# Kernel optimization log

Measured on AMD Instinct MI355X. Metric: run time of the kernel, lower is better.

Reference implementation:

```python
import jax, jax.numpy as jnp
import numpy as np
from jax import lax

B, C, H, W, NH = 16, 512, 32, 32, 8
HC = C // NH  # head channels = 64


def setup_inputs() -> dict:
    key = jax.random.key(0)
    ks = jax.random.split(key, 8)
    rn = lambda i, shape, scale: jax.random.normal(ks[i], shape, jnp.float32) * scale
    return dict(
        image=jax.random.normal(ks[0], (B, C, H, W), jnp.float32),
        watermark=jax.random.normal(ks[1], (B, C, H, W), jnp.float32),
        img_ln_w=jnp.ones((C, H, W), jnp.float32),
        img_ln_b=jnp.zeros((C, H, W), jnp.float32),
        wm_ln_w=jnp.ones((C, H, W), jnp.float32),
        wm_ln_b=jnp.zeros((C, H, W), jnp.float32),
        img_pw_w=rn(2, (3 * C, C), 0.02),
        img_pw_b=jnp.zeros((3 * C,), jnp.float32),
        img_dw_w=rn(3, (3 * C, 3, 3, 3), 0.1),
        img_dw_b=jnp.zeros((3 * C,), jnp.float32),
        wm_pw_w=rn(4, (3 * C, C), 0.02),
        wm_pw_b=jnp.zeros((3 * C,), jnp.float32),
        wm_dw_w=rn(5, (3 * C, 3, 3, 3), 0.1),
        wm_dw_b=jnp.zeros((3 * C,), jnp.float32),
        proj=rn(6, (2 * C, C), 0.02),
    )


def _layernorm(x, w, b, eps=1e-5):
    # LayerNorm over [C,H,W] per sample, elementwise affine of shape [C,H,W]
    mu = jnp.mean(x, axis=(1, 2, 3), keepdims=True)
    var = jnp.mean((x - mu) ** 2, axis=(1, 2, 3), keepdims=True)
    return (x - mu) * lax.rsqrt(var + eps) * w + b


def _dconv_proj(x, pw_w, pw_b, dw_w, dw_b):
    # pointwise 1x1 conv C -> 3C
    x = jnp.einsum('bchw,oc->bohw', x, pw_w) + pw_b[None, :, None, None]
    # depthwise 3x3 conv on 3C channels with groups=C (3 channels per group)
    x = lax.conv_general_dilated(
        x, dw_w, window_strides=(1, 1), padding='SAME',
        dimension_numbers=('NCHW', 'OIHW', 'NCHW'), feature_group_count=C)
    x = x + dw_b[None, :, None, None]
    return jnp.split(x, 3, axis=1)  # Q, K, V each [B,C,H,W]


def reference(image, watermark, img_ln_w, img_ln_b, wm_ln_w, wm_ln_b,
              img_pw_w, img_pw_b, img_dw_w, img_dw_b,
              wm_pw_w, wm_pw_b, wm_dw_w, wm_dw_b, proj):
    img = _layernorm(image, img_ln_w, img_ln_b)
    wm = _layernorm(watermark, wm_ln_w, wm_ln_b)
    Qi, Ki, Vi = _dconv_proj(img, img_pw_w, img_pw_b, img_dw_w, img_dw_b)
    Qw, Kw, Vw = _dconv_proj(wm, wm_pw_w, wm_pw_b, wm_dw_w, wm_dw_b)
    r = lambda t: t.reshape(B, NH, HC, H * W)
    Qi, Ki, Vi, Qw, Kw, Vw = map(r, (Qi, Ki, Vi, Qw, Kw, Vw))
    # NOTE: original code calls F.normalize but discards the result -> no-op.
    Kc = jnp.concatenate([Ki, Kw], axis=2)  # [B,NH,2*HC,HW]
    Vc = jnp.concatenate([Vi, Vw], axis=2)  # [B,NH,2*HC,HW]
    # scores: K_concat @ Q^T over the HW axis -> [B,NH,2*HC,HC], softmax over HC
    Ai = jax.nn.softmax(jnp.einsum('bnkp,bnqp->bnkq', Kc, Qi), axis=-1)
    Aw = jax.nn.softmax(jnp.einsum('bnkp,bnqp->bnkq', Kc, Qw), axis=-1)
    # A^T @ V_concat -> [B,NH,HC,HW]
    img_attn = jnp.einsum('bnkq,bnkp->bnqp', Ai, Vc)
    wm_attn = jnp.einsum('bnkq,bnkp->bnqp', Aw, Vc)
    attn = jnp.concatenate([img_attn, wm_attn], axis=2).reshape(B, 2 * C, H, W)
    # final channel-mixing projection: [B,H,W,2C] @ [2C,C] -> [B,C,H,W]
    return jnp.einsum('bdhw,dc->bchw', attn, proj)
```

## Files before the change

### kernel.cpp

```cpp
#include <hip/hip_runtime.h>
#include <hip/hip_bf16.h>
#include <stdint.h>

#define Bn  16
#define Cch 512
#define C3  1536
#define HWp 1024

typedef __attribute__((ext_vector_type(8))) short bf16x8;
typedef __attribute__((ext_vector_type(4))) float f32x4;

#define DEV static __device__ __forceinline__

DEV float bflo(unsigned u) { return __builtin_bit_cast(float, u << 16); }
DEV float bfhi(unsigned u) { return __builtin_bit_cast(float, u & 0xffff0000u); }
DEV unsigned short f2bf(float f) {
  __hip_bfloat16 h = __float2bfloat16(f);
  return __builtin_bit_cast(unsigned short, h);
}

DEV void async16(__hip_bfloat16* lds, const __hip_bfloat16* g) {
  __builtin_amdgcn_global_load_lds(
      (const __attribute__((address_space(1))) unsigned*)g,
      (__attribute__((address_space(3))) unsigned*)lds, 16, 0, 0);
}

__global__ __launch_bounds__(256) void k_prep_ln(
    const float* __restrict__ img_pw_w, const float* __restrict__ wm_pw_w,
    const float* __restrict__ proj,
    const float* __restrict__ image, const float* __restrict__ watermark,
    __hip_bfloat16* __restrict__ Wpw, __hip_bfloat16* __restrict__ projT,
    float* __restrict__ part)
{
  __shared__ float ls[4], lss[4];
  int blkid = blockIdx.x;
  if (blkid < 8192) {
    int i = blkid * 256 + threadIdx.x;
    const int NW = C3 * Cch;
    if (i < NW)          Wpw[i] = __float2bfloat16(img_pw_w[i]);
    else if (i < 2 * NW) Wpw[i] = __float2bfloat16(wm_pw_w[i - NW]);
    else {
      int j = i - 2 * NW;
      int c = j >> 10, d = j & 1023;
      projT[(size_t)c * 1024 + d] = __float2bfloat16(proj[(size_t)d * 512 + c]);
    }
    return;
  }
  int blk = blkid - 8192;
  int chunk = blk & 63, b = (blk >> 6) & 15, t = blk >> 10;
  const float* x = (t ? watermark : image) + (size_t)b * Cch * HWp + chunk * 8192;
  const float4* xv = (const float4*)x;
  float s = 0.f, ss = 0.f;
#pragma unroll
  for (int i = 0; i < 8; i++) {
    float4 v = xv[threadIdx.x + i * 256];
    s  += v.x + v.y + v.z + v.w;
    ss += v.x * v.x + v.y * v.y + v.z * v.z + v.w * v.w;
  }
#pragma unroll
  for (int off = 32; off; off >>= 1) { s += __shfl_down(s, off); ss += __shfl_down(ss, off); }
  int wv = threadIdx.x >> 6;
  if ((threadIdx.x & 63) == 0) { ls[wv] = s; lss[wv] = ss; }
  __syncthreads();
  if (threadIdx.x == 0) {
    part[blk * 2]     = ls[0] + ls[1] + ls[2] + ls[3];
    part[blk * 2 + 1] = lss[0] + lss[1] + lss[2] + lss[3];
  }
}

__global__ void k_ln_final(const float* __restrict__ part, float* __restrict__ stats)
{
  int i = threadIdx.x;
  if (i < 32) {
    float S = 0.f, SS = 0.f;
    for (int c2 = 0; c2 < 64; c2++) { S += part[(i * 64 + c2) * 2]; SS += part[(i * 64 + c2) * 2 + 1]; }
    const float inv = 1.f / (float)(Cch * HWp);
    float mu  = S * inv;
    float var = SS * inv - mu * mu;
    stats[i]      = mu;
    stats[32 + i] = rsqrtf(var + 1e-5f);
  }
}

__global__ __launch_bounds__(256) void k_norm_t(
    const float* __restrict__ image, const float* __restrict__ watermark,
    const float* __restrict__ img_w, const float* __restrict__ img_b,
    const float* __restrict__ wm_w,  const float* __restrict__ wm_b,
    const float* __restrict__ stats, __hip_bfloat16* __restrict__ xnT)
{
  int blk = blockIdx.x;
  int ct = blk & 15, pt = (blk >> 4) & 15, b = (blk >> 8) & 15, t = blk >> 12;
  int c0 = ct * 32, p0 = pt * 64;
  const float* x   = (t ? watermark : image) + (size_t)b * Cch * HWp;
  const float* wgt = t ? wm_w : img_w;
  const float* bia = t ? wm_b : img_b;
  float mu = stats[t * 16 + b], rstd = stats[32 + t * 16 + b];
  __shared__ float tile[32 * 66];
  int tid = threadIdx.x;
  {
    int c = tid >> 3, s = tid & 7;
    const float* xr = x   + (size_t)(c0 + c) * HWp + p0;
    const float* wr = wgt + (size_t)(c0 + c) * HWp + p0;
    const float* br = bia + (size_t)(c0 + c) * HWp + p0;
#pragma unroll
    for (int j = 0; j < 2; j++) {
      int f = s + j * 8;
      float4 xv = *(const float4*)&xr[f * 4];
      float4 wv = *(const float4*)&wr[f * 4];
      float4 bv = *(const float4*)&br[f * 4];
      float n0 = (xv.x - mu) * rstd * wv.x + bv.x;
      float n1 = (xv.y - mu) * rstd * wv.y + bv.y;
      float n2 = (xv.z - mu) * rstd * wv.z + bv.z;
      float n3 = (xv.w - mu) * rstd * wv.w + bv.w;
      *(float2*)&tile[c * 66 + f * 4]     = make_float2(n0, n1);
      *(float2*)&tile[c * 66 + f * 4 + 2] = make_float2(n2, n3);
    }
  }
  __syncthreads();
  {
    int p = tid >> 2, cq = tid & 3;
    union { unsigned short us[8]; uint4 v4; } pk;
#pragma unroll
    for (int j = 0; j < 8; j++) pk.us[j] = f2bf(tile[(cq * 8 + j) * 66 + p]);
    __hip_bfloat16* dst = xnT + ((size_t)(t * 16 + b)) * HWp * Cch
                        + (size_t)(p0 + p) * Cch + c0 + cq * 8;
    *(uint4*)dst = pk.v4;
  }
}

template<int MI, int Kdim, int Ncols, bool OBF, bool HB>
DEV void gemm_core(const __hip_bfloat16* __restrict__ A,
                   const __hip_bfloat16* __restrict__ Bt,
                   const float* __restrict__ bias, void* __restrict__ Cout)
{
  constexpr int MT = MI * 32;
  __shared__ __hip_bfloat16 As[MT * 64];
  __shared__ __hip_bfloat16 Bs[128 * 64];
  const int tid = threadIdx.x, lane = tid & 63, wv = tid >> 6;
  const int lr = lane & 15, lq = lane >> 4;
  const int wm = (wv >> 1) * (MI * 16), wn = (wv & 1) * 64;
  const int m0 = blockIdx.y * MT, n0 = blockIdx.x * 128;
  f32x4 acc[MI][4] = {};
  const int srow = tid >> 3, sslot = tid & 7;
  const int sseg = (sslot ^ (srow & 7)) * 8;
  for (int k0 = 0; k0 < Kdim; k0 += 64) {
#pragma unroll
    for (int c = 0; c < MI; c++) {
      int row = srow + c * 32;
      async16(&As[row * 64 + sslot * 8], &A[(size_t)(m0 + row) * Kdim + k0 + sseg]);
    }
#pragma unroll
    for (int c = 0; c < 4; c++) {
      int row = srow + c * 32;
      async16(&Bs[row * 64 + sslot * 8], &Bt[(size_t)(n0 + row) * Kdim + k0 + sseg]);
    }
    __syncthreads();
#pragma unroll
    for (int ks = 0; ks < 2; ks++) {
      bf16x8 af[MI], bfr[4];
#pragma unroll
      for (int mi = 0; mi < MI; mi++) {
        int r = wm + mi * 16 + lr;
        af[mi]  = *(const bf16x8*)&As[r * 64 + (((ks * 4 + lq) ^ (lr & 7)) * 8)];
      }
#pragma unroll
      for (int ni = 0; ni < 4; ni++) {
        int r = wn + ni * 16 + lr;
        bfr[ni] = *(const bf16x8*)&Bs[r * 64 + (((ks * 4 + lq) ^ (lr & 7)) * 8)];
      }
#pragma unroll
      for (int mi = 0; mi < MI; mi++)
#pragma unroll
        for (int ni = 0; ni < 4; ni++)
          acc[mi][ni] = __builtin_amdgcn_mfma_f32_16x16x32_bf16(af[mi], bfr[ni], acc[mi][ni], 0, 0, 0);
    }
    __syncthreads();
  }
#pragma unroll
  for (int mi = 0; mi < MI; mi++) {
    int mrow = m0 + wm + mi * 16 + lq * 4;
#pragma unroll
    for (int ni = 0; ni < 4; ni++) {
      int ncol = n0 + wn + ni * 16 + lr;
#pragma unroll
      for (int r = 0; r < 4; r++) {
        float y = acc[mi][ni][r];
        int row = mrow + r;
        if (HB) y += bias[row];
        if (OBF) ((__hip_bfloat16*)Cout)[(size_t)row * Ncols + ncol] = __float2bfloat16(y);
        else     ((float*)Cout)[(size_t)row * Ncols + ncol] = y;
      }
    }
  }
}

__global__ __launch_bounds__(256) void k_pw_gemm(
    const __hip_bfloat16* __restrict__ Wpw, const __hip_bfloat16* __restrict__ xnT,
    const float* __restrict__ img_pw_b, const float* __restrict__ wm_pw_b,
    __hip_bfloat16* __restrict__ Y)
{
  int bz = blockIdx.z, t = bz >> 4;
  gemm_core<4, 512, 1024, true, true>(
      Wpw + (size_t)t * C3 * Cch,
      xnT + (size_t)bz * HWp * Cch,
      t ? wm_pw_b : img_pw_b,
      Y + (size_t)bz * C3 * HWp);
}

__global__ __launch_bounds__(256) void k_proj_gemm(
    const __hip_bfloat16* __restrict__ projT, const __hip_bfloat16* __restrict__ attnT,
    float* __restrict__ out)
{
  int b = blockIdx.z;
  gemm_core<2, 1024, 1024, false, false>(
      projT, attnT + (size_t)b * HWp * 1024, nullptr, out + (size_t)b * Cch * HWp);
}

__global__ __launch_bounds__(256) void k_dw(
    const __hip_bfloat16* __restrict__ Y,
    const float* __restrict__ img_dw_w, const float* __restrict__ img_dw_b,
    const float* __restrict__ wm_dw_w,  const float* __restrict__ wm_dw_b,
    __hip_bfloat16* __restrict__ QKV)
{
  int idx = blockIdx.x * 256 + threadIdx.x;
  int w0 = (idx & 3) * 8;
  int h  = (idx >> 2) & 31;
  int g  = __builtin_amdgcn_readfirstlane((idx >> 7) & 511);
  int tb = __builtin_amdgcn_readfirstlane(idx >> 16);
  int t  = tb >> 4;
  const float* dww = (t ? wm_dw_w : img_dw_w) + g * 81;
  const float* dwb = (t ? wm_dw_b : img_dw_b) + g * 3;
  const __hip_bfloat16* base = Y + ((size_t)tb * C3 + g * 3) * HWp;
  float acc[3][8];
#pragma unroll
  for (int o = 0; o < 3; o++) {
    float bv = dwb[o];
#pragma unroll
    for (int w = 0; w < 8; w++) acc[o][w] = bv;
  }
  const bool mlo = (w0 == 0), mhi = (w0 == 24);
#pragma unroll
  for (int i = 0; i < 3; i++) {
#pragma unroll
    for (int kh = 0; kh < 3; kh++) {
      int hh = h + kh - 1;
      if ((unsigned)hh > 31u) continue;
      const unsigned* up = (const unsigned*)(base + i * HWp + hh * 32 + (w0 - 2));
      float v[12];
#pragma unroll
      for (int d2 = 0; d2 < 6; d2++) { unsigned u = up[d2]; v[d2*2] = bflo(u); v[d2*2+1] = bfhi(u); }
      if (mlo) { v[0] = 0.f; v[1] = 0.f; }
      if (mhi) { v[10] = 0.f; v[11] = 0.f; }
#pragma unroll
      for (int o = 0; o < 3; o++) {
        float wk0 = dww[o*27 + i*9 + kh*3 + 0];
        float wk1 = dww[o*27 + i*9 + kh*3 + 1];
        float wk2 = dww[o*27 + i*9 + kh*3 + 2];
#pragma unroll
        for (int w = 0; w < 8; w++)
          acc[o][w] += v[w + 1] * wk0 + v[w + 2] * wk1 + v[w + 3] * wk2;
      }
    }
  }
#pragma unroll
  for (int o = 0; o < 3; o++) {
    union { unsigned short us[8]; uint4 v4; } pk;
#pragma unroll
    for (int w = 0; w < 8; w++) pk.us[w] = f2bf(acc[o][w]);
    *(uint4*)(QKV + ((size_t)tb * C3 + g * 3 + o) * HWp + h * 32 + w0) = pk.v4;
  }
}

__global__ __launch_bounds__(256) void k_attn_scores(
    const __hip_bfloat16* __restrict__ QKV, __hip_bfloat16* __restrict__ ATg)
{
  int blk = blockIdx.x, kh = blk & 1, m = (blk >> 1) & 1, bn = blk >> 2;
  int b = bn >> 3, nh = bn & 7;
  int tid = threadIdx.x, lane = tid & 63, wv = tid >> 6;
  int lr = lane & 15, lq = lane >> 4;
  const __hip_bfloat16* kb =
      QKV + (((size_t)(kh * 16 + b)) * C3 + 512 + nh * 64 + (wv * 16 + lr)) * HWp + lq * 8;
  const __hip_bfloat16* qbase[4];
#pragma unroll
  for (int qt = 0; qt < 4; qt++)
    qbase[qt] = QKV + (((size_t)(m * 16 + b)) * C3 + nh * 64 + qt * 16 + lr) * HWp + lq * 8;

  f32x4 acc[4] = {};
  for (int p0 = 0; p0 < HWp; p0 += 32) {
    bf16x8 bk = *(const bf16x8*)(kb + p0);
#pragma unroll
    for (int qt = 0; qt < 4; qt++) {
      bf16x8 aq = *(const bf16x8*)(qbase[qt] + p0);
      acc[qt] = __builtin_amdgcn_mfma_f32_16x16x32_bf16(aq, bk, acc[qt], 0, 0, 0);
    }
  }
  __shared__ float S[64][65];
  __shared__ float redmax[4][64];
  __shared__ float redsum[4][64];
  __shared__ __hip_bfloat16 Ash[64][72];
#pragma unroll
  for (int qt = 0; qt < 4; qt++)
#pragma unroll
    for (int r = 0; r < 4; r++)
      S[qt * 16 + lq * 4 + r][wv * 16 + lr] = acc[qt][r];
  __syncthreads();
  int k = tid & 63, sub = tid >> 6;
  float vals[16], mx = -1e30f;
#pragma unroll
  for (int j = 0; j < 16; j++) { vals[j] = S[sub * 16 + j][k]; mx = fmaxf(mx, vals[j]); }
  redmax[sub][k] = mx;
  __syncthreads();
  float M = fmaxf(fmaxf(redmax[0][k], redmax[1][k]), fmaxf(redmax[2][k], redmax[3][k]));
  float ssum = 0.f;
#pragma unroll
  for (int j = 0; j < 16; j++) { vals[j] = __expf(vals[j] - M); ssum += vals[j]; }
  redsum[sub][k] = ssum;
  __syncthreads();
  float inv = 1.f / (redsum[0][k] + redsum[1][k] + redsum[2][k] + redsum[3][k]);
#pragma unroll
  for (int j = 0; j < 16; j++) Ash[sub * 16 + j][k] = __float2bfloat16(vals[j] * inv);
  __syncthreads();
  __hip_bfloat16* outp = ATg + ((size_t)(bn * 2 + m)) * 64 * 128 + kh * 64;
#pragma unroll
  for (int s = 0; s < 2; s++) {
    int id = tid + s * 256, row = id >> 3, seg = (id & 7) * 8;
    *(uint4*)&outp[(size_t)row * 128 + seg] = *(const uint4*)&Ash[row][seg];
  }
}

__global__ __launch_bounds__(256) void k_attn_out(
    const __hip_bfloat16* __restrict__ QKV, const __hip_bfloat16* __restrict__ ATg,
    __hip_bfloat16* __restrict__ attnT)
{
  int blk = blockIdx.x, pc = blk & 3, bn = blk >> 2, b = bn >> 3, nh = bn & 7;
  int tid = threadIdx.x, lane = tid & 63, wv = tid >> 6;
  int lr = lane & 15, lq = lane >> 4;
  __shared__ __hip_bfloat16 ATs[2][64][136];
  __shared__ __hip_bfloat16 VTs[64][136];
#pragma unroll
  for (int m = 0; m < 2; m++) {
    const __hip_bfloat16* src = ATg + ((size_t)(bn * 2 + m)) * 64 * 128;
#pragma unroll
    for (int s = 0; s < 4; s++) {
      int id = tid + s * 256, row = id >> 4, seg = (id & 15) * 8;
      *(uint4*)&ATs[m][row][seg] = *(const uint4*)&src[row * 128 + seg];
    }
  }
  const int vk0 = (tid >> 3) * 4, vps = (tid & 7) * 8;
  for (int ps = 0; ps < 4; ps++) {
    int p0 = pc * 256 + ps * 64;
    __syncthreads();
    union { uint4 v4; unsigned short us[8]; } ld[4];
#pragma unroll
    for (int j = 0; j < 4; j++) {
      int kk = vk0 + j, tk = kk >> 6, hc = kk & 63;
      ld[j].v4 = *(const uint4*)(QKV +
          (((size_t)(tk * 16 + b)) * C3 + 1024 + nh * 64 + hc) * HWp + p0 + vps);
    }
#pragma unroll
    for (int e = 0; e < 8; e++) {
      uint2 w;
      w.x = (unsigned)ld[0].us[e] | ((unsigned)ld[1].us[e] << 16);
      w.y = (unsigned)ld[2].us[e] | ((unsigned)ld[3].us[e] << 16);
      *(uint2*)&VTs[vps + e][vk0] = w;
    }
    __syncthreads();
#pragma unroll
    for (int m = 0; m < 2; m++) {
      f32x4 oacc[4] = {};
#pragma unroll
      for (int ks = 0; ks < 4; ks++) {
        bf16x8 bv = *(const bf16x8*)&VTs[wv * 16 + lr][ks * 32 + lq * 8];
#pragma unroll
        for (int qt = 0; qt < 4; qt++) {
          bf16x8 av = *(const bf16x8*)&ATs[m][qt * 16 + lr][ks * 32 + lq * 8];
          oacc[qt] = __builtin_amdgcn_mfma_f32_16x16x32_bf16(av, bv, oacc[qt], 0, 0, 0);
        }
      }
#pragma unroll
      for (int qt = 0; qt < 4; qt++) {
        int q = qt * 16 + lq * 4;
        int d = nh * 128 + m * 64 + q;
        int p = p0 + wv * 16 + lr;
        union { unsigned short us[4]; uint2 v2; } pk;
#pragma unroll
        for (int r = 0; r < 4; r++) pk.us[r] = f2bf(oacc[qt][r]);
        *(uint2*)&attnT[((size_t)b * HWp + p) * 1024 + d] = pk.v2;
      }
    }
  }
}

extern "C" void kernel_launch(void* const* d_in, const int* in_sizes, int n_in,
                              void* d_out, int out_size, void* d_ws, size_t ws_size,
                              hipStream_t stream)
{
  (void)in_sizes; (void)n_in; (void)out_size; (void)ws_size;
  const float* image     = (const float*)d_in[0];
  const float* watermark = (const float*)d_in[1];
  const float* img_ln_w  = (const float*)d_in[2];
  const float* img_ln_b  = (const float*)d_in[3];
  const float* wm_ln_w   = (const float*)d_in[4];
  const float* wm_ln_b   = (const float*)d_in[5];
  const float* img_pw_w  = (const float*)d_in[6];
  const float* img_pw_b  = (const float*)d_in[7];
  const float* img_dw_w  = (const float*)d_in[8];
  const float* img_dw_b  = (const float*)d_in[9];
  const float* wm_pw_w   = (const float*)d_in[10];
  const float* wm_pw_b   = (const float*)d_in[11];
  const float* wm_dw_w   = (const float*)d_in[12];
  const float* wm_dw_b   = (const float*)d_in[13];
  const float* proj      = (const float*)d_in[14];

  char* ws = (char*)d_ws;
  __hip_bfloat16* Wpw    = (__hip_bfloat16*)(ws + 0);
  __hip_bfloat16* projT  = (__hip_bfloat16*)(ws + 3145728);
  float*          lnpart = (float*)(ws + 4194304);
  float*          stats  = (float*)(ws + 4210688);
  __hip_bfloat16* xnT    = (__hip_bfloat16*)(ws + 5242880);
  __hip_bfloat16* attnT  = xnT;
  __hip_bfloat16* Y      = (__hip_bfloat16*)(ws + 41943040);
  __hip_bfloat16* ATg    = Y;
  __hip_bfloat16* QKV    = (__hip_bfloat16*)(ws + 142606336);

  k_prep_ln<<<10240, 256, 0, stream>>>(img_pw_w, wm_pw_w, proj, image, watermark,
                                       Wpw, projT, lnpart);
  k_ln_final<<<1, 64, 0, stream>>>(lnpart, stats);
  k_norm_t<<<8192, 256, 0, stream>>>(image, watermark, img_ln_w, img_ln_b,
                                     wm_ln_w, wm_ln_b, stats, xnT);
  dim3 gpw(8, 12, 32);
  k_pw_gemm<<<gpw, 256, 0, stream>>>(Wpw, xnT, img_pw_b, wm_pw_b, Y);
  k_dw<<<8192, 256, 0, stream>>>(Y, img_dw_w, img_dw_b, wm_dw_w, wm_dw_b, QKV);
  k_attn_scores<<<512, 256, 0, stream>>>(QKV, ATg);
  k_attn_out<<<512, 256, 0, stream>>>(QKV, ATg, attnT);
  dim3 gpj(8, 8, 16);
  k_proj_gemm<<<gpj, 256, 0, stream>>>(projT, attnT, (float*)d_out);
}
```

Measured before the change: 364.3 us.

## Fuse attention score softmax with output GEMM and fold LN stats into normalize

Merges the attention scores/softmax kernel and the attention-output kernel into one kernel. Each block computes the full 128-key score matrix for its query set and keeps the softmax weights in shared memory, so the global ATg round trip and one launch go away. The price is that each block recomputes the full score GEMM for its half of the positions, duplicating that work across the two halves. Separately, the single-block LN-finalize kernel is removed and every normalize block reduces the 64 partial sums itself, saving a serialized tiny launch at the cost of redundant reductions.

```diff
diff --git a/kernel.cpp b/kernel.cpp
--- a/kernel.cpp
+++ b/kernel.cpp
@@ -68,25 +68,11 @@
   }
 }
 
-__global__ void k_ln_final(const float* __restrict__ part, float* __restrict__ stats)
-{
-  int i = threadIdx.x;
-  if (i < 32) {
-    float S = 0.f, SS = 0.f;
-    for (int c2 = 0; c2 < 64; c2++) { S += part[(i * 64 + c2) * 2]; SS += part[(i * 64 + c2) * 2 + 1]; }
-    const float inv = 1.f / (float)(Cch * HWp);
-    float mu  = S * inv;
-    float var = SS * inv - mu * mu;
-    stats[i]      = mu;
-    stats[32 + i] = rsqrtf(var + 1e-5f);
-  }
-}
-
 __global__ __launch_bounds__(256) void k_norm_t(
     const float* __restrict__ image, const float* __restrict__ watermark,
     const float* __restrict__ img_w, const float* __restrict__ img_b,
     const float* __restrict__ wm_w,  const float* __restrict__ wm_b,
-    const float* __restrict__ stats, __hip_bfloat16* __restrict__ xnT)
+    const float* __restrict__ part, __hip_bfloat16* __restrict__ xnT)
 {
   int blk = blockIdx.x;
   int ct = blk & 15, pt = (blk >> 4) & 15, b = (blk >> 8) & 15, t = blk >> 12;
@@ -94,9 +80,23 @@
   const float* x   = (t ? watermark : image) + (size_t)b * Cch * HWp;
   const float* wgt = t ? wm_w : img_w;
   const float* bia = t ? wm_b : img_b;
-  float mu = stats[t * 16 + b], rstd = stats[32 + t * 16 + b];
+  __shared__ float stt[2];
+  int tid = threadIdx.x;
+  if (tid < 64) {
+    float2 pr = ((const float2*)part)[t * 1024 + b * 64 + tid];
+    float s = pr.x, ss = pr.y;
+#pragma unroll
+    for (int off = 32; off; off >>= 1) { s += __shfl_down(s, off); ss += __shfl_down(ss, off); }
+    if (tid == 0) {
+      const float inv = 1.f / (float)(Cch * HWp);
+      float mu = s * inv;
+      float var = ss * inv - mu * mu;
+      stt[0] = mu; stt[1] = rsqrtf(var + 1e-5f);
+    }
+  }
+  __syncthreads();
+  float mu = stt[0], rstd = stt[1];
   __shared__ float tile[32 * 66];
-  int tid = threadIdx.x;
   {
     int c = tid >> 3, s = tid & 7;
     const float* xr = x   + (size_t)(c0 + c) * HWp + p0;
@@ -271,84 +271,69 @@
   }
 }
 
-__global__ __launch_bounds__(256) void k_attn_scores(
-    const __hip_bfloat16* __restrict__ QKV, __hip_bfloat16* __restrict__ ATg)
-{
-  int blk = blockIdx.x, kh = blk & 1, m = (blk >> 1) & 1, bn = blk >> 2;
+__global__ __launch_bounds__(256) void k_attn(
+    const __hip_bfloat16* __restrict__ QKV, __hip_bfloat16* __restrict__ attnT)
+{
+  int blk = blockIdx.x, ph = blk & 1, m = (blk >> 1) & 1, bn = blk >> 2;
   int b = bn >> 3, nh = bn & 7;
   int tid = threadIdx.x, lane = tid & 63, wv = tid >> 6;
   int lr = lane & 15, lq = lane >> 4;
-  const __hip_bfloat16* kb =
-      QKV + (((size_t)(kh * 16 + b)) * C3 + 512 + nh * 64 + (wv * 16 + lr)) * HWp + lq * 8;
+
+  const __hip_bfloat16* kb[2];
+#pragma unroll
+  for (int kt = 0; kt < 2; kt++)
+    kb[kt] = QKV + (((size_t)(kt * 16 + b)) * C3 + 512 + nh * 64 + (wv * 16 + lr)) * HWp + lq * 8;
   const __hip_bfloat16* qbase[4];
 #pragma unroll
   for (int qt = 0; qt < 4; qt++)
     qbase[qt] = QKV + (((size_t)(m * 16 + b)) * C3 + nh * 64 + qt * 16 + lr) * HWp + lq * 8;
 
-  f32x4 acc[4] = {};
+  f32x4 acc[2][4] = {};
   for (int p0 = 0; p0 < HWp; p0 += 32) {
-    bf16x8 bk = *(const bf16x8*)(kb + p0);
+    bf16x8 bk[2];
+#pragma unroll
+    for (int kt = 0; kt < 2; kt++) bk[kt] = *(const bf16x8*)(kb[kt] + p0);
 #pragma unroll
     for (int qt = 0; qt < 4; qt++) {
       bf16x8 aq = *(const bf16x8*)(qbase[qt] + p0);
-      acc[qt] = __builtin_amdgcn_mfma_f32_16x16x32_bf16(aq, bk, acc[qt], 0, 0, 0);
-    }
-  }
-  __shared__ float S[64][65];
-  __shared__ float redmax[4][64];
-  __shared__ float redsum[4][64];
-  __shared__ __hip_bfloat16 Ash[64][72];
-#pragma unroll
-  for (int qt = 0; qt < 4; qt++)
-#pragma unroll
-    for (int r = 0; r < 4; r++)
-      S[qt * 16 + lq * 4 + r][wv * 16 + lr] = acc[qt][r];
-  __syncthreads();
-  int k = tid & 63, sub = tid >> 6;
-  float vals[16], mx = -1e30f;
-#pragma unroll
-  for (int j = 0; j < 16; j++) { vals[j] = S[sub * 16 + j][k]; mx = fmaxf(mx, vals[j]); }
-  redmax[sub][k] = mx;
-  __syncthreads();
-  float M = fmaxf(fmaxf(redmax[0][k], redmax[1][k]), fmaxf(redmax[2][k], redmax[3][k]));
+#pragma unroll
+      for (int kt = 0; kt < 2; kt++)
+        acc[kt][qt] = __builtin_amdgcn_mfma_f32_16x16x32_bf16(aq, bk[kt], acc[kt][qt], 0, 0, 0);
+    }
+  }
+
+  __shared__ float S[64][129];
+  __shared__ float red[2][2][128];
+  __shared__ __hip_bfloat16 ATs[64][136];
+  __shared__ __hip_bfloat16 VTs[64][136];
+#pragma unroll
+  for (int kt = 0; kt < 2; kt++)
+#pragma unroll
+    for (int qt = 0; qt < 4; qt++)
+#pragma unroll
+      for (int r = 0; r < 4; r++)
+        S[qt * 16 + lq * 4 + r][kt * 64 + wv * 16 + lr] = acc[kt][qt][r];
+  __syncthreads();
+
+  int k = tid & 127, half = tid >> 7;
+  float vals[32], mx = -1e30f;
+#pragma unroll
+  for (int j = 0; j < 32; j++) { vals[j] = S[half * 32 + j][k]; mx = fmaxf(mx, vals[j]); }
+  red[0][half][k] = mx;
+  __syncthreads();
+  float M = fmaxf(red[0][0][k], red[0][1][k]);
   float ssum = 0.f;
 #pragma unroll
-  for (int j = 0; j < 16; j++) { vals[j] = __expf(vals[j] - M); ssum += vals[j]; }
-  redsum[sub][k] = ssum;
-  __syncthreads();
-  float inv = 1.f / (redsum[0][k] + redsum[1][k] + redsum[2][k] + redsum[3][k]);
-#pragma unroll
-  for (int j = 0; j < 16; j++) Ash[sub * 16 + j][k] = __float2bfloat16(vals[j] * inv);
-  __syncthreads();
-  __hip_bfloat16* outp = ATg + ((size_t)(bn * 2 + m)) * 64 * 128 + kh * 64;
-#pragma unroll
-  for (int s = 0; s < 2; s++) {
-    int id = tid + s * 256, row = id >> 3, seg = (id & 7) * 8;
-    *(uint4*)&outp[(size_t)row * 128 + seg] = *(const uint4*)&Ash[row][seg];
-  }
-}
-
-__global__ __launch_bounds__(256) void k_attn_out(
-    const __hip_bfloat16* __restrict__ QKV, const __hip_bfloat16* __restrict__ ATg,
-    __hip_bfloat16* __restrict__ attnT)
-{
-  int blk = blockIdx.x, pc = blk & 3, bn = blk >> 2, b = bn >> 3, nh = bn & 7;
-  int tid = threadIdx.x, lane = tid & 63, wv = tid >> 6;
-  int lr = lane & 15, lq = lane >> 4;
-  __shared__ __hip_bfloat16 ATs[2][64][136];
-  __shared__ __hip_bfloat16 VTs[64][136];
-#pragma unroll
-  for (int m = 0; m < 2; m++) {
-    const __hip_bfloat16* src = ATg + ((size_t)(bn * 2 + m)) * 64 * 128;
-#pragma unroll
-    for (int s = 0; s < 4; s++) {
-      int id = tid + s * 256, row = id >> 4, seg = (id & 15) * 8;
-      *(uint4*)&ATs[m][row][seg] = *(const uint4*)&src[row * 128 + seg];
-    }
-  }
+  for (int j = 0; j < 32; j++) { vals[j] = __expf(vals[j] - M); ssum += vals[j]; }
+  red[1][half][k] = ssum;
+  __syncthreads();
+  float inv = 1.f / (red[1][0][k] + red[1][1][k]);
+#pragma unroll
+  for (int j = 0; j < 32; j++) ATs[half * 32 + j][k] = __float2bfloat16(vals[j] * inv);
+
   const int vk0 = (tid >> 3) * 4, vps = (tid & 7) * 8;
-  for (int ps = 0; ps < 4; ps++) {
-    int p0 = pc * 256 + ps * 64;
+  for (int ps = 0; ps < 8; ps++) {
+    int p0 = ph * 512 + ps * 64;
     __syncthreads();
     union { uint4 v4; unsigned short us[8]; } ld[4];
 #pragma unroll
@@ -365,28 +350,25 @@
       *(uint2*)&VTs[vps + e][vk0] = w;
     }
     __syncthreads();
-#pragma unroll
-    for (int m = 0; m < 2; m++) {
-      f32x4 oacc[4] = {};
-#pragma unroll
-      for (int ks = 0; ks < 4; ks++) {
-        bf16x8 bv = *(const bf16x8*)&VTs[wv * 16 + lr][ks * 32 + lq * 8];
-#pragma unroll
-        for (int qt = 0; qt < 4; qt++) {
-          bf16x8 av = *(const bf16x8*)&ATs[m][qt * 16 + lr][ks * 32 + lq * 8];
-          oacc[qt] = __builtin_amdgcn_mfma_f32_16x16x32_bf16(av, bv, oacc[qt], 0, 0, 0);
-        }
+    f32x4 oacc[4] = {};
+#pragma unroll
+    for (int ks = 0; ks < 4; ks++) {
+      bf16x8 bv = *(const bf16x8*)&VTs[wv * 16 + lr][ks * 32 + lq * 8];
+#pragma unroll
+      for (int qt = 0; qt < 4; qt++) {
+        bf16x8 av = *(const bf16x8*)&ATs[qt * 16 + lr][ks * 32 + lq * 8];
+        oacc[qt] = __builtin_amdgcn_mfma_f32_16x16x32_bf16(av, bv, oacc[qt], 0, 0, 0);
       }
-#pragma unroll
-      for (int qt = 0; qt < 4; qt++) {
-        int q = qt * 16 + lq * 4;
-        int d = nh * 128 + m * 64 + q;
-        int p = p0 + wv * 16 + lr;
-        union { unsigned short us[4]; uint2 v2; } pk;
-#pragma unroll
-        for (int r = 0; r < 4; r++) pk.us[r] = f2bf(oacc[qt][r]);
-        *(uint2*)&attnT[((size_t)b * HWp + p) * 1024 + d] = pk.v2;
-      }
+    }
+#pragma unroll
+    for (int qt = 0; qt < 4; qt++) {
+      int q = qt * 16 + lq * 4;
+      int d = nh * 128 + m * 64 + q;
+      int p = p0 + wv * 16 + lr;
+      union { unsigned short us[4]; uint2 v2; } pk;
+#pragma unroll
+      for (int r = 0; r < 4; r++) pk.us[r] = f2bf(oacc[qt][r]);
+      *(uint2*)&attnT[((size_t)b * HWp + p) * 1024 + d] = pk.v2;
     }
   }
 }
@@ -416,23 +398,19 @@
   __hip_bfloat16* Wpw    = (__hip_bfloat16*)(ws + 0);
   __hip_bfloat16* projT  = (__hip_bfloat16*)(ws + 3145728);
   float*          lnpart = (float*)(ws + 4194304);
-  float*          stats  = (float*)(ws + 4210688);
   __hip_bfloat16* xnT    = (__hip_bfloat16*)(ws + 5242880);
   __hip_bfloat16* attnT  = xnT;
   __hip_bfloat16* Y      = (__hip_bfloat16*)(ws + 41943040);
-  __hip_bfloat16* ATg    = Y;
   __hip_bfloat16* QKV    = (__hip_bfloat16*)(ws + 142606336);
 
   k_prep_ln<<<10240, 256, 0, stream>>>(img_pw_w, wm_pw_w, proj, image, watermark,
                                        Wpw, projT, lnpart);
-  k_ln_final<<<1, 64, 0, stream>>>(lnpart, stats);
   k_norm_t<<<8192, 256, 0, stream>>>(image, watermark, img_ln_w, img_ln_b,
-                                     wm_ln_w, wm_ln_b, stats, xnT);
+                                     wm_ln_w, wm_ln_b, lnpart, xnT);
   dim3 gpw(8, 12, 32);
   k_pw_gemm<<<gpw, 256, 0, stream>>>(Wpw, xnT, img_pw_b, wm_pw_b, Y);
   k_dw<<<8192, 256, 0, stream>>>(Y, img_dw_w, img_dw_b, wm_dw_w, wm_dw_b, QKV);
-  k_attn_scores<<<512, 256, 0, stream>>>(QKV, ATg);
-  k_attn_out<<<512, 256, 0, stream>>>(QKV, ATg, attnT);
+  k_attn<<<512, 256, 0, stream>>>(QKV, attnT);
   dim3 gpj(8, 8, 16);
   k_proj_gemm<<<gpj, 256, 0, stream>>>(projT, attnT, (float*)d_out);
 }
```

After: 369.7 us. About the same (+1.5%).
